# Kernel tuning notes

Hardware: AMD Instinct MI355X
Metric: run time of the kernel (lower is better)

The kernel has to match this reference:

```python
import jax, jax.numpy as jnp
import numpy as np
from jax import lax

B, T, D = 8, 2048, 1024
DECAY = 0.99
EPS = 1e-5


def _layer_norm(x, w, b):
    mu = jnp.mean(x, axis=-1, keepdims=True)
    var = jnp.var(x, axis=-1, keepdims=True)
    return (x - mu) * lax.rsqrt(var + EPS) * w + b


def _fixed_decay_scan(v, decay):
    # h_t = decay * h_{t-1} + v_t along axis=1, h_0 = v_0 (zero initial state)
    a = jnp.full_like(v, decay)

    def combine(c1, c2):
        a1, b1 = c1
        a2, b2 = c2
        return (a1 * a2, a2 * b1 + b2)

    _, h = lax.associative_scan(combine, (a, v), axis=1)
    return h


def setup_inputs() -> dict:
    key = jax.random.key(0)
    ks = jax.random.split(key, 12)
    s = 0.02
    return {
        "x": jax.random.normal(ks[0], (B, T, D), dtype=jnp.float32),
        "mask": jnp.ones((B, T), dtype=jnp.float32),
        "ln1_w": jnp.ones((D,), jnp.float32),
        "ln1_b": jnp.zeros((D,), jnp.float32),
        "ln2_w": jnp.ones((D,), jnp.float32),
        "ln2_b": jnp.zeros((D,), jnp.float32),
        "Wg_f": jax.random.normal(ks[1], (D, D), jnp.float32) * s,
        "bg_f": jnp.ones((D,), jnp.float32),
        "Wg_b": jax.random.normal(ks[2], (D, D), jnp.float32) * s,
        "bg_b": jnp.ones((D,), jnp.float32),
        "W_fuse": jax.random.normal(ks[3], (2 * D, D), jnp.float32) * s,
        "b_fuse": jnp.zeros((D,), jnp.float32),
        "W_ffn1": jax.random.normal(ks[4], (D, 2 * D), jnp.float32) * s,
        "b_ffn1": jnp.zeros((2 * D,), jnp.float32),
        "W_ffn2": jax.random.normal(ks[5], (2 * D, D), jnp.float32) * s,
        "b_ffn2": jnp.zeros((D,), jnp.float32),
    }


def reference(x, mask, ln1_w, ln1_b, ln2_w, ln2_b, Wg_f, bg_f, Wg_b, bg_b,
              W_fuse, b_fuse, W_ffn1, b_ffn1, W_ffn2, b_ffn2):
    residual = x
    h = _layer_norm(x, ln1_w, ln1_b)
    m = mask[..., None]  # (B,T,1)

    # forward-direction gated scan
    v_fwd = jax.nn.sigmoid(h @ Wg_f + bg_f) * h * m
    h_fwd = _fixed_decay_scan(v_fwd, DECAY)

    # backward-direction gated scan (scan over reversed time)
    v_bwd = jax.nn.sigmoid(h @ Wg_b + bg_b) * h * m
    h_bwd = jnp.flip(_fixed_decay_scan(jnp.flip(v_bwd, axis=1), DECAY), axis=1)

    # learned fusion gate
    beta = jax.nn.sigmoid(jnp.concatenate([h_fwd, h_bwd], axis=-1) @ W_fuse + b_fuse)
    fused = beta * h_fwd + (1.0 - beta) * h_bwd

    x = residual + fused  # dropout is identity in eval mode

    # FFN block (exact GELU as torch nn.GELU default)
    ffn = jax.nn.gelu(_layer_norm(x, ln2_w, ln2_b) @ W_ffn1 + b_ffn1, approximate=False) @ W_ffn2 + b_ffn2
    return x + ffn
```

## Files before the change

kernel.cpp:

```cpp
#include <hip/hip_runtime.h>
#include <math.h>

#define Bq 8
#define Tq 2048
#define Dq 1024
#define Mq (Bq*Tq)
#define NCHq 32
#define CHUNKq 64
#define DECAYq 0.99f
#define DF64q 0.52559646f
#define SG2q (Bq*NCHq*2)
#define CEBNDq ((size_t)Bq*NCHq*Dq)

typedef unsigned short u16;
typedef unsigned int u32;
typedef __attribute__((ext_vector_type(8))) short bf16x8;
typedef __attribute__((ext_vector_type(4))) float f32x4;
typedef __attribute__((ext_vector_type(4))) u16 u16x4;

__device__ __forceinline__ u16 f2bf(float f) {
  u32 u = __builtin_bit_cast(u32, f);
  return (u16)((u + 0x7FFFu + ((u >> 16) & 1u)) >> 16);
}
__device__ __forceinline__ float bf2f(u16 h) {
  return __builtin_bit_cast(float, (u32)h << 16);
}
__device__ __forceinline__ float sigm(float x) { return 1.0f / (1.0f + expf(-x)); }

__global__ __launch_bounds__(256)
void transpose_all(const float* __restrict__ s0, u16* __restrict__ d0,
                   const float* __restrict__ s1, u16* __restrict__ d1,
                   const float* __restrict__ s2, u16* __restrict__ d2,
                   const float* __restrict__ s3, u16* __restrict__ d3,
                   const float* __restrict__ s4, u16* __restrict__ d4) {
  const int bid = blockIdx.x;
  const float* src; u16* dst; int K, N, local;
  if (bid < 1024)      { src = s0; dst = d0; K = 1024; N = 1024; local = bid; }
  else if (bid < 2048) { src = s1; dst = d1; K = 1024; N = 1024; local = bid - 1024; }
  else if (bid < 4096) { src = s2; dst = d2; K = 2048; N = 1024; local = bid - 2048; }
  else if (bid < 6144) { src = s3; dst = d3; K = 1024; N = 2048; local = bid - 4096; }
  else                 { src = s4; dst = d4; K = 2048; N = 1024; local = bid - 6144; }
  const int ntx = N >> 5;
  const int n0 = (local % ntx) << 5;
  const int k0 = (local / ntx) << 5;
  __shared__ float tile[32][33];
  const int tx = threadIdx.x & 31;
  const int ty = threadIdx.x >> 5;
#pragma unroll
  for (int j = 0; j < 32; j += 8)
    tile[ty + j][tx] = src[(size_t)(k0 + ty + j) * N + (n0 + tx)];
  __syncthreads();
#pragma unroll
  for (int j = 0; j < 32; j += 8)
    dst[(size_t)(n0 + ty + j) * K + (k0 + tx)] = f2bf(tile[tx][ty + j]);
}

__global__ __launch_bounds__(256)
void ln_kernel(const float* __restrict__ xin, const float* __restrict__ w,
               const float* __restrict__ bb, u16* __restrict__ obf) {
  const int row = blockIdx.x;
  const int tid = threadIdx.x;
  const float4 v = ((const float4*)(xin + (size_t)row * Dq))[tid];
  float s  = v.x + v.y + v.z + v.w;
  float s2 = v.x*v.x + v.y*v.y + v.z*v.z + v.w*v.w;
#pragma unroll
  for (int o = 32; o > 0; o >>= 1) { s += __shfl_xor(s, o); s2 += __shfl_xor(s2, o); }
  __shared__ float rs[4], rq[4];
  const int wid = tid >> 6;
  if ((tid & 63) == 0) { rs[wid] = s; rq[wid] = s2; }
  __syncthreads();
  s  = rs[0] + rs[1] + rs[2] + rs[3];
  s2 = rq[0] + rq[1] + rq[2] + rq[3];
  const float mu  = s * (1.0f/Dq);
  const float var = s2 * (1.0f/Dq) - mu*mu;
  const float inv = rsqrtf(var + 1e-5f);
  const float4 wv = ((const float4*)w)[tid];
  const float4 bv = ((const float4*)bb)[tid];
  float4 o;
  o.x = (v.x - mu)*inv*wv.x + bv.x;
  o.y = (v.y - mu)*inv*wv.y + bv.y;
  o.z = (v.z - mu)*inv*wv.z + bv.z;
  o.w = (v.w - mu)*inv*wv.w + bv.w;
  u16x4 ob; ob[0] = f2bf(o.x); ob[1] = f2bf(o.y); ob[2] = f2bf(o.z); ob[3] = f2bf(o.w);
  ((u16x4*)(obf + (size_t)row * Dq))[tid] = ob;
}

__global__ __launch_bounds__(256)
void ln_bf_kernel(const u16* __restrict__ xin, const float* __restrict__ w,
                  const float* __restrict__ bb, u16* __restrict__ obf) {
  const int row = blockIdx.x;
  const int tid = threadIdx.x;
  const u16x4 vu = ((const u16x4*)(xin + (size_t)row * Dq))[tid];
  float v0 = bf2f(vu[0]), v1 = bf2f(vu[1]), v2 = bf2f(vu[2]), v3 = bf2f(vu[3]);
  float s  = v0 + v1 + v2 + v3;
  float s2 = v0*v0 + v1*v1 + v2*v2 + v3*v3;
#pragma unroll
  for (int o = 32; o > 0; o >>= 1) { s += __shfl_xor(s, o); s2 += __shfl_xor(s2, o); }
  __shared__ float rs[4], rq[4];
  const int wid = tid >> 6;
  if ((tid & 63) == 0) { rs[wid] = s; rq[wid] = s2; }
  __syncthreads();
  s  = rs[0] + rs[1] + rs[2] + rs[3];
  s2 = rq[0] + rq[1] + rq[2] + rq[3];
  const float mu  = s * (1.0f/Dq);
  const float var = s2 * (1.0f/Dq) - mu*mu;
  const float inv = rsqrtf(var + 1e-5f);
  const float4 wv = ((const float4*)w)[tid];
  const float4 bv = ((const float4*)bb)[tid];
  u16x4 ob;
  ob[0] = f2bf((v0 - mu)*inv*wv.x + bv.x);
  ob[1] = f2bf((v1 - mu)*inv*wv.y + bv.y);
  ob[2] = f2bf((v2 - mu)*inv*wv.z + bv.z);
  ob[3] = f2bf((v3 - mu)*inv*wv.w + bv.w);
  ((u16x4*)(obf + (size_t)row * Dq))[tid] = ob;
}

__global__ __launch_bounds__(256)
void scan_pass1_dual(const u32* __restrict__ vf, const u32* __restrict__ vb,
                     float* __restrict__ ce) {
  int bid = blockIdx.x;
  const bool rev = bid >= SG2q;
  if (rev) bid -= SG2q;
  const int dp = ((bid & 1) << 8) + threadIdx.x;
  const int c  = (bid >> 1) & 31;
  const int b  = bid >> 6;
  const u32* v = rev ? vb : vf;
  float* cep   = ce + (rev ? CEBNDq : 0);
  const long step = rev ? -(long)512 : (long)512;
  size_t idx = ((size_t)b * Tq + (rev ? (Tq - 1 - c * CHUNKq) : c * CHUNKq)) * 512 + dp;
  float e0 = 0.0f, e1 = 0.0f;
  for (int i = 0; i < CHUNKq; ++i) {
    const u32 pv = v[idx];
    e0 = DECAYq * e0 + bf2f((u16)(pv & 0xffffu));
    e1 = DECAYq * e1 + bf2f((u16)(pv >> 16));
    idx += step;
  }
  float2* o = (float2*)(cep + ((size_t)b * NCHq + c) * Dq + ((size_t)dp << 1));
  *o = make_float2(e0, e1);
}

__global__ __launch_bounds__(256)
void scan_pass2_dual(const float* __restrict__ ce, float* __restrict__ car) {
  const int idx = blockIdx.x * 256 + threadIdx.x;
  const int dir = idx >> 13;
  const int loc = idx & 8191;
  const int b = loc >> 10;
  const int d = loc & 1023;
  const size_t base = (size_t)dir * CEBNDq;
  float c = 0.0f;
  for (int k = 0; k < NCHq; ++k) {
    const size_t i = base + ((size_t)b * NCHq + k) * Dq + d;
    car[i] = c;
    c = DF64q * c + ce[i];
  }
}

__global__ __launch_bounds__(256)
void scan_pass3_dual(u32* __restrict__ vf, u32* __restrict__ vb,
                     const float* __restrict__ car) {
  int bid = blockIdx.x;
  const bool rev = bid >= SG2q;
  if (rev) bid -= SG2q;
  const int dp = ((bid & 1) << 8) + threadIdx.x;
  const int c  = (bid >> 1) & 31;
  const int b  = bid >> 6;
  u32* v = rev ? vb : vf;
  const float* carp = car + (rev ? CEBNDq : 0);
  const float2 c2 = *(const float2*)(carp + ((size_t)b * NCHq + c) * Dq + ((size_t)dp << 1));
  float h0 = c2.x, h1 = c2.y;
  const long step = rev ? -(long)512 : (long)512;
  size_t idx = ((size_t)b * Tq + (rev ? (Tq - 1 - c * CHUNKq) : c * CHUNKq)) * 512 + dp;
  for (int i = 0; i < CHUNKq; ++i) {
    const u32 pv = v[idx];
    h0 = DECAYq * h0 + bf2f((u16)(pv & 0xffffu));
    h1 = DECAYq * h1 + bf2f((u16)(pv >> 16));
    v[idx] = (u32)f2bf(h0) | ((u32)f2bf(h1) << 16);
    idx += step;
  }
}

struct EpiGate {
  const u16* h; const float* mask; const float* bgf; const float* bgb;
  u16* vf; u16* vb;
  __device__ void operator()(int r, int c, float val) const {
    const bool fwd = c < 1024;
    const int cc = c & 1023;
    const float s = sigm(val + (fwd ? bgf[cc] : bgb[cc]));
    const float hv = bf2f(h[(size_t)r * Dq + cc]) * mask[r];
    (fwd ? vf : vb)[(size_t)r * Dq + cc] = f2bf(s * hv);
  }
};
struct EpiFuse {
  const float* bfuse; const float* x; const u16* hf; const u16* hb; u16* x2;
  __device__ void operator()(int r, int c, float val) const {
    const size_t i = (size_t)r * Dq + c;
    const float bta = sigm(val + bfuse[c]);
    x2[i] = f2bf(x[i] + bta * bf2f(hf[i]) + (1.0f - bta) * bf2f(hb[i]));
  }
};
struct EpiFfn1 {
  const float* b1; u16* a;
  __device__ void operator()(int r, int c, float val) const {
    const float u = val + b1[c];
    const float g = 0.5f * u * (1.0f + erff(u * 0.70710678118f));
    a[(size_t)r * 2048 + c] = f2bf(g);
  }
};
struct EpiFfn2 {
  const float* b2; const u16* x2; float* o;
  __device__ void operator()(int r, int c, float val) const {
    const size_t i = (size_t)r * Dq + c;
    o[i] = val + b2[c] + bf2f(x2[i]);
  }
};

template<typename Epi>
__global__ __launch_bounds__(512)
void gemm_bt(const u16* __restrict__ A, const u16* __restrict__ A2, int ksplit,
             const u16* __restrict__ BT, int K, int nx, Epi epi) {
  __shared__ u16 As[2][8192];
  __shared__ u16 Bs[2][8192];
  const int tid  = threadIdx.x;
  const int lane = tid & 63;
  const int w    = tid >> 6;
  const int wr   = w >> 2;
  const int wc   = w & 3;

  const int lin = blockIdx.x;
  const int q8  = gridDim.x >> 3;
  const int t   = (lin & 7) * q8 + (lin >> 3);
  const int by  = t / nx;
  const int bx  = t - by * nx;
  const int rowBase = by << 7;
  const int colBase = bx << 7;

  const int srow  = tid >> 3;
  const int scolE = (((tid & 7) ^ (srow & 7)) << 4) >> 1;
  const int KA    = (ksplit < K) ? ksplit : K;

  auto stage = [&](int buf, int kt) {
    const int kbase = kt << 6;
    const u16* Abase = (kbase < ksplit) ? A : A2;
    const int  kA    = (kbase < ksplit) ? kbase : (kbase - ksplit);
#pragma unroll
    for (int qq = 0; qq < 2; ++qq) {
      const u16* ga = Abase + (size_t)(rowBase + (qq << 6) + srow) * KA + kA + scolE;
      const u16* gb = BT    + (size_t)(colBase + (qq << 6) + srow) * K + kbase + scolE;
      __builtin_amdgcn_global_load_lds(
          (const __attribute__((address_space(1))) void*)ga,
          (__attribute__((address_space(3))) void*)(&As[buf][0] + (qq << 12) + (w << 9)), 16, 0, 0);
      __builtin_amdgcn_global_load_lds(
          (const __attribute__((address_space(1))) void*)gb,
          (__attribute__((address_space(3))) void*)(&Bs[buf][0] + (qq << 12) + (w << 9)), 16, 0, 0);
    }
  };

  f32x4 acc[4][2];
#pragma unroll
  for (int m = 0; m < 4; ++m)
#pragma unroll
    for (int n = 0; n < 2; ++n) acc[m][n] = (f32x4){0.f, 0.f, 0.f, 0.f};

  const int nkt = K >> 6;
  stage(0, 0);
  asm volatile("s_waitcnt vmcnt(0)" ::: "memory");
  __builtin_amdgcn_s_barrier();

  int cur = 0;
  for (int kt = 0; kt < nkt; ++kt) {
    if (kt + 1 < nkt) stage(cur ^ 1, kt + 1);
    const char* Ab = (const char*)&As[cur][0];
    const char* Bb = (const char*)&Bs[cur][0];
#pragma unroll
    for (int kk = 0; kk < 2; ++kk) {
      bf16x8 af[4], bfr[2];
      const int cb = (kk << 6) + ((lane >> 4) << 4);
#pragma unroll
      for (int m = 0; m < 4; ++m) {
        const int r = (wr << 6) + (m << 4) + (lane & 15);
        af[m] = *(const bf16x8*)(Ab + (r << 7) + (cb ^ ((r & 7) << 4)));
      }
#pragma unroll
      for (int n = 0; n < 2; ++n) {
        const int r = (wc << 5) + (n << 4) + (lane & 15);
        bfr[n] = *(const bf16x8*)(Bb + (r << 7) + (cb ^ ((r & 7) << 4)));
      }
#pragma unroll
      for (int m = 0; m < 4; ++m)
#pragma unroll
        for (int n = 0; n < 2; ++n)
          acc[m][n] = __builtin_amdgcn_mfma_f32_16x16x32_bf16(af[m], bfr[n], acc[m][n], 0, 0, 0);
    }
    __builtin_amdgcn_sched_barrier(0);
    asm volatile("s_waitcnt vmcnt(0) lgkmcnt(0)" ::: "memory");
    __builtin_amdgcn_s_barrier();
    cur ^= 1;
  }

#pragma unroll
  for (int m = 0; m < 4; ++m) {
    const int grow0 = rowBase + (wr << 6) + (m << 4) + ((lane >> 4) << 2);
#pragma unroll
    for (int n = 0; n < 2; ++n) {
      const int gcol = colBase + (wc << 5) + (n << 4) + (lane & 15);
#pragma unroll
      for (int r2 = 0; r2 < 4; ++r2)
        epi(grow0 + r2, gcol, acc[m][n][r2]);
    }
  }
}

extern "C" void kernel_launch(void* const* d_in, const int* in_sizes, int n_in,
                              void* d_out, int out_size, void* d_ws, size_t ws_size,
                              hipStream_t stream) {
  (void)in_sizes; (void)n_in; (void)out_size; (void)ws_size;
  const float* x      = (const float*)d_in[0];
  const float* mask   = (const float*)d_in[1];
  const float* ln1w   = (const float*)d_in[2];
  const float* ln1b   = (const float*)d_in[3];
  const float* ln2w   = (const float*)d_in[4];
  const float* ln2b   = (const float*)d_in[5];
  const float* Wg_f   = (const float*)d_in[6];
  const float* bg_f   = (const float*)d_in[7];
  const float* Wg_b   = (const float*)d_in[8];
  const float* bg_b   = (const float*)d_in[9];
  const float* W_fuse = (const float*)d_in[10];
  const float* b_fuse = (const float*)d_in[11];
  const float* W_ffn1 = (const float*)d_in[12];
  const float* b_ffn1 = (const float*)d_in[13];
  const float* W_ffn2 = (const float*)d_in[14];
  const float* b_ffn2 = (const float*)d_in[15];
  float* out = (float*)d_out;

  char* ws = (char*)d_ws;
  size_t off = 0;
  auto alloc = [&](size_t bytes) { char* p = ws + off; off += (bytes + 255) & ~(size_t)255; return p; };
  u16*   x2     = (u16*)  alloc((size_t)Mq * Dq * 2);
  u16*   slotA  = (u16*)  alloc((size_t)Mq * Dq * 2);
  u16*   hf_bf  = (u16*)  alloc((size_t)Mq * Dq * 2);
  u16*   hb_bf  = (u16*)  alloc((size_t)Mq * Dq * 2);
  u16*   WgT    = (u16*)  alloc((size_t)2048 * 1024 * 2);
  u16*   WfuT   = (u16*)  alloc((size_t)1024 * 2048 * 2);
  u16*   Wf1T   = (u16*)  alloc((size_t)2048 * 1024 * 2);
  u16*   Wf2T   = (u16*)  alloc((size_t)1024 * 2048 * 2);
  float* ce     = (float*)alloc(2 * CEBNDq * 4);
  float* car    = (float*)alloc(2 * CEBNDq * 4);
  u16*   h_bf16 = slotA;
  u16*   y2     = slotA;
  u16*   a_bf16 = hf_bf;

  transpose_all<<<8192, 256, 0, stream>>>(Wg_f, WgT, Wg_b, WgT + 1024 * 1024,
                                          W_fuse, WfuT, W_ffn1, Wf1T, W_ffn2, Wf2T);

  ln_kernel<<<Mq, 256, 0, stream>>>(x, ln1w, ln1b, h_bf16);

  EpiGate eg{h_bf16, mask, bg_f, bg_b, hf_bf, hb_bf};
  gemm_bt<EpiGate><<<16 * (Mq / 128), 512, 0, stream>>>(h_bf16, h_bf16, 1024, WgT, 1024, 16, eg);

  scan_pass1_dual<<<2 * SG2q, 256, 0, stream>>>((const u32*)hf_bf, (const u32*)hb_bf, ce);
  scan_pass2_dual<<<64, 256, 0, stream>>>(ce, car);
  scan_pass3_dual<<<2 * SG2q, 256, 0, stream>>>((u32*)hf_bf, (u32*)hb_bf, car);

  EpiFuse ef{b_fuse, x, hf_bf, hb_bf, x2};
  gemm_bt<EpiFuse><<<8 * (Mq / 128), 512, 0, stream>>>(hf_bf, hb_bf, 1024, WfuT, 2048, 8, ef);

  ln_bf_kernel<<<Mq, 256, 0, stream>>>(x2, ln2w, ln2b, y2);

  EpiFfn1 e1{b_ffn1, a_bf16};
  gemm_bt<EpiFfn1><<<16 * (Mq / 128), 512, 0, stream>>>(y2, y2, 1024, Wf1T, 1024, 16, e1);

  EpiFfn2 e2{b_ffn2, x2, out};
  gemm_bt<EpiFfn2><<<8 * (Mq / 128), 512, 0, stream>>>(a_bf16, a_bf16, 2048, Wf2T, 2048, 8, e2);
}
```

Before: 500.4 us.

## Triple-buffer A tiles in GEMM to prefetch two k-steps ahead

Splits the GEMM tile staging into separate A and B loads. A tiles get a third LDS buffer and are prefetched two k-iterations ahead, while B stays double-buffered one step ahead. The end-of-iteration wait changes from a full vmcnt(0) drain to vmcnt(2), so the newest A prefetch can remain in flight across the barrier and more global-load latency is hidden. LDS per block rises from 64KB to 80KB, which may limit how many blocks fit on a CU.

```diff
diff --git a/kernel.cpp b/kernel.cpp
--- a/kernel.cpp
+++ b/kernel.cpp
@@ -218,7 +218,7 @@
 __global__ __launch_bounds__(512)
 void gemm_bt(const u16* __restrict__ A, const u16* __restrict__ A2, int ksplit,
              const u16* __restrict__ BT, int K, int nx, Epi epi) {
-  __shared__ u16 As[2][8192];
+  __shared__ u16 As[3][8192];
   __shared__ u16 Bs[2][8192];
   const int tid  = threadIdx.x;
   const int lane = tid & 63;
@@ -238,17 +238,23 @@
   const int scolE = (((tid & 7) ^ (srow & 7)) << 4) >> 1;
   const int KA    = (ksplit < K) ? ksplit : K;
 
-  auto stage = [&](int buf, int kt) {
+  auto stageA = [&](int buf, int kt) {
     const int kbase = kt << 6;
     const u16* Abase = (kbase < ksplit) ? A : A2;
     const int  kA    = (kbase < ksplit) ? kbase : (kbase - ksplit);
 #pragma unroll
     for (int qq = 0; qq < 2; ++qq) {
       const u16* ga = Abase + (size_t)(rowBase + (qq << 6) + srow) * KA + kA + scolE;
-      const u16* gb = BT    + (size_t)(colBase + (qq << 6) + srow) * K + kbase + scolE;
       __builtin_amdgcn_global_load_lds(
           (const __attribute__((address_space(1))) void*)ga,
           (__attribute__((address_space(3))) void*)(&As[buf][0] + (qq << 12) + (w << 9)), 16, 0, 0);
+    }
+  };
+  auto stageB = [&](int buf, int kt) {
+    const int kbase = kt << 6;
+#pragma unroll
+    for (int qq = 0; qq < 2; ++qq) {
+      const u16* gb = BT + (size_t)(colBase + (qq << 6) + srow) * K + kbase + scolE;
       __builtin_amdgcn_global_load_lds(
           (const __attribute__((address_space(1))) void*)gb,
           (__attribute__((address_space(3))) void*)(&Bs[buf][0] + (qq << 12) + (w << 9)), 16, 0, 0);
@@ -262,15 +268,22 @@
     for (int n = 0; n < 2; ++n) acc[m][n] = (f32x4){0.f, 0.f, 0.f, 0.f};
 
   const int nkt = K >> 6;
-  stage(0, 0);
-  asm volatile("s_waitcnt vmcnt(0)" ::: "memory");
+  stageB(0, 0);
+  stageA(0, 0);
+  if (nkt > 1) {
+    stageA(1, 1);
+    asm volatile("s_waitcnt vmcnt(2)" ::: "memory");
+  } else {
+    asm volatile("s_waitcnt vmcnt(0)" ::: "memory");
+  }
   __builtin_amdgcn_s_barrier();
 
-  int cur = 0;
+  int ab = 0, bb = 0;
   for (int kt = 0; kt < nkt; ++kt) {
-    if (kt + 1 < nkt) stage(cur ^ 1, kt + 1);
-    const char* Ab = (const char*)&As[cur][0];
-    const char* Bb = (const char*)&Bs[cur][0];
+    if (kt + 1 < nkt) stageB(bb ^ 1, kt + 1);
+    if (kt + 2 < nkt) stageA(ab ? ab - 1 : 2, kt + 2);
+    const char* Ab = (const char*)&As[ab][0];
+    const char* Bb = (const char*)&Bs[bb][0];
 #pragma unroll
     for (int kk = 0; kk < 2; ++kk) {
       bf16x8 af[4], bfr[2];
@@ -292,9 +305,12 @@
           acc[m][n] = __builtin_amdgcn_mfma_f32_16x16x32_bf16(af[m], bfr[n], acc[m][n], 0, 0, 0);
     }
     __builtin_amdgcn_sched_barrier(0);
-    asm volatile("s_waitcnt vmcnt(0) lgkmcnt(0)" ::: "memory");
+    asm volatile("s_waitcnt lgkmcnt(0)" ::: "memory");
+    if (kt + 2 < nkt) asm volatile("s_waitcnt vmcnt(2)" ::: "memory");
+    else              asm volatile("s_waitcnt vmcnt(0)" ::: "memory");
     __builtin_amdgcn_s_barrier();
-    cur ^= 1;
+    ab = (ab == 2) ? 0 : ab + 1;
+    bb ^= 1;
   }
 
 #pragma unroll
```

Result: no change. 501.2 us (+0.1%).
